# Kernel tuning notes

Hardware: AMD Instinct MI355X
Metric: run time of the kernel (lower is better)

## Reference

```python
import jax, jax.numpy as jnp
import numpy as np

N, E = 100000, 1600000
DIM, H, D = 64, 4, 8          # dim, num_heads, qk_dim
DH = D * H                    # 32
QK_SCALE = (DIM // H) ** -0.5


def setup_inputs() -> dict:
    key = jax.random.key(0)
    k1, k2, k3, k4 = jax.random.split(key, 4)
    x = jax.random.normal(k1, (N, DIM), dtype=jnp.float32)
    edge_index = jax.random.randint(k2, (2, E), 0, N, dtype=jnp.int64)
    W_qkv = jax.random.normal(k3, (DIM, 2 * DH + DIM), dtype=jnp.float32) * (DIM ** -0.5)
    b_qkv = jax.random.normal(k4, (2 * DH + DIM,), dtype=jnp.float32) * 0.02
    return {"x": x, "edge_index": edge_index, "W_qkv": W_qkv, "b_qkv": b_qkv}


def reference(x, edge_index, W_qkv, b_qkv):
    n = x.shape[0]
    e = edge_index.shape[1]
    qkv = x @ W_qkv + b_qkv                       # (N, 2*DH+DIM)
    q = qkv[:, :DH].reshape(n, H, D)
    k = qkv[:, DH:2 * DH].reshape(n, H, D)
    v = qkv[:, 2 * DH:].reshape(n, H, DIM // H)
    s, t = edge_index[0], edge_index[1]
    q_e = q[s] * QK_SCALE                         # (E, H, D)
    k_e = k[t]
    v_e = v[t]                                    # (E, H, DIM/H)
    # scale q by 1/sqrt(num source neighbors) (bincount of s)
    deg = jax.ops.segment_sum(jnp.ones((e,), x.dtype), s, num_segments=n)
    q_e = q_e * (deg[s] ** -0.5)[:, None, None]
    compat = jnp.einsum('ehd,ehd->eh', q_e, k_e)  # (E, H)
    # segment softmax over edges grouped by source node s
    m = jax.ops.segment_max(compat, s, num_segments=n)
    ex = jnp.exp(compat - m[s])
    denom = jax.ops.segment_sum(ex, s, num_segments=n)
    attn = ex / (denom[s] + 1e-16)                # (E, H)
    msg = (v_e * attn[..., None]).reshape(e, DIM)  # (E, DIM)
    out = jax.ops.segment_sum(msg, s, num_segments=n)  # (N, DIM)
    return out
```

## Files before the change

### kernel.cpp

```cpp
#include <hip/hip_runtime.h>


#define NDIM 64
#define NBMAX 1024
#define CTILE 8192
#define STGMAX 4352
#define GEMM_BLKS 316

static __device__ __forceinline__ unsigned short f2bf(float f) {
    unsigned int u = __float_as_uint(f);
    unsigned int r = (u + 0x7fffu + ((u >> 16) & 1u)) >> 16;
    return (unsigned short)r;
}
static __device__ __forceinline__ float bflo(unsigned int u) {
    return __uint_as_float(u << 16);
}
static __device__ __forceinline__ float bfhi(unsigned int u) {
    return __uint_as_float(u & 0xffff0000u);
}

__global__ void fused_bin_gemm_kernel(const int* __restrict__ s_arr,
                                      const int* __restrict__ t_arr,
                                      unsigned int* __restrict__ gcur,
                                      unsigned int* __restrict__ binned,
                                      const float* __restrict__ x,
                                      const float* __restrict__ W,
                                      const float* __restrict__ bvec,
                                      unsigned short* __restrict__ qs16,
                                      unsigned short* __restrict__ kv,
                                      int N, int E, int nbin) {
    __shared__ unsigned int sm[2048];
    int tid = threadIdx.x;

    if (blockIdx.x < (unsigned)nbin) {
        unsigned int* hist  = sm;
        unsigned int* gbase = sm + 1024;
        int e0 = blockIdx.x * CTILE;
        int cnt = min(CTILE, E - e0);

        hist[tid] = 0;
        __syncthreads();
        for (int i = tid; i < cnt; i += 1024)
            atomicAdd(&hist[(unsigned)s_arr[e0 + i] >> 7], 1u);
        __syncthreads();
        {
            unsigned int h = hist[tid];
            gbase[tid] = h
                ? (unsigned)tid * STGMAX + atomicAdd(&gcur[tid], h)
                : 0u;
        }
        __syncthreads();
        for (int i = tid; i < cnt; i += 1024) {
            int s = s_arr[e0 + i];
            int t = t_arr[e0 + i];
            unsigned int bkt = (unsigned)s >> 7;
            unsigned int dst = atomicAdd(&gbase[bkt], 1u);
            if (dst < (bkt + 1u) * STGMAX)
                binned[dst] = ((unsigned)(s & 127) << 17) | (unsigned)t;
        }
    } else {
        float4* xs = (float4*)sm;
        int bid = blockIdx.x - nbin;
        int col = tid & 127;
        int rw  = tid >> 7;
        float w[64];
        #pragma unroll
        for (int k = 0; k < 64; ++k) w[k] = W[k * 128 + col];
        float bias = bvec[col];

        for (int r0 = bid * 8; r0 < N; r0 += GEMM_BLKS * 8) {
            __syncthreads();
            if (tid < 128) {
                int rr = tid >> 4;
                int cc = tid & 15;
                int n = r0 + rr;
                xs[rr * 16 + cc] = (n < N)
                    ? reinterpret_cast<const float4*>(x)[(size_t)n * 16 + cc]
                    : make_float4(0.f, 0.f, 0.f, 0.f);
            }
            __syncthreads();
            int n = r0 + rw;
            if (n < N) {
                float acc = bias;
                #pragma unroll
                for (int k4 = 0; k4 < 16; ++k4) {
                    float4 xv = xs[rw * 16 + k4];
                    acc = fmaf(xv.x, w[4 * k4 + 0], acc);
                    acc = fmaf(xv.y, w[4 * k4 + 1], acc);
                    acc = fmaf(xv.z, w[4 * k4 + 2], acc);
                    acc = fmaf(xv.w, w[4 * k4 + 3], acc);
                }
                if (col < 32) {
                    qs16[(size_t)n * 32 + col] = f2bf(acc);
                } else if (col < 64) {
                    kv[(size_t)n * 96 + (col - 32)] = f2bf(acc);
                } else {
                    kv[(size_t)n * 96 + 32 + (col - 64)] = f2bf(acc);
                }
            }
        }
    }
}

__global__ void __launch_bounds__(512, 8)
sort_aggregate_kernel(const unsigned int* __restrict__ gcur,
                      const unsigned int* __restrict__ binned,
                      const unsigned short* __restrict__ qs16,
                      const unsigned int* __restrict__ kv32,
                      float* __restrict__ out, int N) {
    __shared__ unsigned int hist[128];
    __shared__ unsigned int rstart[128];
    __shared__ unsigned int cur[128];
    __shared__ unsigned int sh[128];
    __shared__ unsigned int stg[STGMAX];

    int b = blockIdx.x;
    int tid = threadIdx.x;
    unsigned int base = (unsigned)b * STGMAX;
    unsigned int cnt = min(gcur[b], (unsigned int)STGMAX);

    if (tid < 128) hist[tid] = 0;
    __syncthreads();
    for (unsigned int i = tid; i < cnt; i += 512)
        atomicAdd(&hist[binned[base + i] >> 17], 1u);
    __syncthreads();

    unsigned int v = (tid < 128) ? hist[tid] : 0;
    unsigned int acc = v;
    if (tid < 128) sh[tid] = acc;
    __syncthreads();
    for (int o = 1; o < 128; o <<= 1) {
        unsigned int add = (tid >= o && tid < 128) ? sh[tid - o] : 0;
        __syncthreads();
        if (tid < 128) { acc += add; sh[tid] = acc; }
        __syncthreads();
    }
    if (tid < 128) {
        unsigned int exc = acc - v;
        rstart[tid] = exc;
        cur[tid] = exc;
    }
    __syncthreads();

    for (unsigned int i = tid; i < cnt; i += 512) {
        unsigned int e = binned[base + i];
        unsigned int p = atomicAdd(&cur[e >> 17], 1u);
        stg[p] = (e & 0x1FFFFu) * 192u;
    }
    __syncthreads();

    int wid = tid >> 6, lane = tid & 63;
    int hl   = lane & 31;
    int sub  = lane >> 5;
    int head = hl >> 3;
    const char* kvb = (const char*)kv32;
    const char* qsb = (const char*)qs16;

    for (int nl = wid * 16; nl < wid * 16 + 16; ++nl) {
        int n = b * 128 + nl;
        if (n >= N) break;
        int dg = (int)hist[nl];
        if (dg == 0) {
            if (lane < 32)
                *reinterpret_cast<float2*>(&out[(size_t)n * 64 + 2 * hl]) =
                    make_float2(0.f, 0.f);
            continue;
        }
        int start = (int)rstart[nl];
        int last = start + dg - 1;
        float sc = 0.25f * rsqrtf((float)dg);

        uint4 q4 = *(const uint4*)(qsb + (size_t)n * 64 + (head << 4));
        float qf0 = bflo(q4.x) * sc, qf1 = bfhi(q4.x) * sc;
        float qf2 = bflo(q4.y) * sc, qf3 = bfhi(q4.y) * sc;
        float qf4 = bflo(q4.z) * sc, qf5 = bfhi(q4.z) * sc;
        float qf6 = bflo(q4.w) * sc, qf7 = bfhi(q4.w) * sc;

        float accx = 0.f, accy = 0.f, den = 0.f;
        int npairs = (dg + 1) >> 1;
        int idx = start + sub;

        unsigned int co = stg[min(idx, last)];
        float wm = (idx <= last) ? 1.f : 0.f;
        uint4 kr = *(const uint4*)(kvb + co + (head << 4));
        unsigned int vr = *(const unsigned int*)(kvb + co + 64 + (hl << 2));

        for (int i = 0; i < npairs; ++i) {
            uint4 kr2 = kr; unsigned int vr2 = vr; float wm2 = 0.f;
            int idx2 = idx + 2;
            if (i + 1 < npairs) {
                unsigned int co2 = stg[min(idx2, last)];
                wm2 = (idx2 <= last) ? 1.f : 0.f;
                kr2 = *(const uint4*)(kvb + co2 + (head << 4));
                vr2 = *(const unsigned int*)(kvb + co2 + 64 + (hl << 2));
            }
            float p = qf0 * bflo(kr.x);
            p = fmaf(qf1, bfhi(kr.x), p);
            p = fmaf(qf2, bflo(kr.y), p);
            p = fmaf(qf3, bfhi(kr.y), p);
            p = fmaf(qf4, bflo(kr.z), p);
            p = fmaf(qf5, bfhi(kr.z), p);
            p = fmaf(qf6, bflo(kr.w), p);
            p = fmaf(qf7, bfhi(kr.w), p);
            float w = __expf(p) * wm;
            accx = fmaf(w, bflo(vr), accx);
            accy = fmaf(w, bfhi(vr), accy);
            den += w;
            kr = kr2; vr = vr2; wm = wm2; idx = idx2;
        }

        accx += __shfl_xor(accx, 32);
        accy += __shfl_xor(accy, 32);
        den  += __shfl_xor(den, 32);

        if (lane < 32) {
            float inv = 1.0f / (den + 1e-16f);
            *reinterpret_cast<float2*>(&out[(size_t)n * 64 + 2 * hl]) =
                make_float2(accx * inv, accy * inv);
        }
    }
}

extern "C" void kernel_launch(void* const* d_in, const int* in_sizes, int n_in,
                              void* d_out, int out_size, void* d_ws, size_t ws_size,
                              hipStream_t stream) {
    const float* x = (const float*)d_in[0];
    const int*   eidx = (const int*)d_in[1];
    const float* W = (const float*)d_in[2];
    const float* b = (const float*)d_in[3];
    int N = in_sizes[0] / NDIM;
    int E = in_sizes[1] / 2;
    float* out = (float*)d_out;

    int NB = (N + 127) / 128;
    int nbin = (E + CTILE - 1) / CTILE;

    unsigned short* qs16 = (unsigned short*)d_ws;
    unsigned short* kv = qs16 + (size_t)N * 32;
    unsigned int* gcur = (unsigned int*)(kv + (size_t)N * 96);
    unsigned int* binned = gcur + NBMAX;

    const int* s_arr = eidx;
    const int* t_arr = eidx + E;

    hipMemsetAsync(gcur, 0, NBMAX * sizeof(unsigned int), stream);

    fused_bin_gemm_kernel<<<nbin + GEMM_BLKS, 1024, 0, stream>>>(
        s_arr, t_arr, gcur, binned, x, W, b, qs16, kv, N, E, nbin);
    sort_aggregate_kernel<<<NB, 512, 0, stream>>>(
        gcur, binned, qs16, (const unsigned int*)kv, out, N);
}
```

Baseline: 183.8 us.

## Split global bin counters into 8 partitions and shrink staging buffer

Binning blocks now write to one of 8 partitions per bucket, chosen by block index, which spreads global atomic contention on the per-bucket counters. Staging capacity per partition is 384 and the aggregate kernel's shared staging array shrinks to 3072 entries to improve occupancy. The scan of bucket counts uses wavefront shuffles instead of a barrier-heavy shared-memory scan. The risk is silently dropped edges when one partition overflows its 384 slots or a bucket exceeds 3072 edges in total.

New measurement: 181.4 us. About the same (-1.3%).

```diff
diff --git a/kernel.cpp b/kernel.cpp
--- a/kernel.cpp
+++ b/kernel.cpp
@@ -4,7 +4,8 @@
 #define NDIM 64
 #define NBMAX 1024
 #define CTILE 8192
-#define STGMAX 4352
+#define STGP 384
+#define STGTOT 3072
 #define GEMM_BLKS 316
 
 static __device__ __forceinline__ unsigned short f2bf(float f) {
@@ -37,6 +38,7 @@
         unsigned int* gbase = sm + 1024;
         int e0 = blockIdx.x * CTILE;
         int cnt = min(CTILE, E - e0);
+        unsigned int part = blockIdx.x & 7u;
 
         hist[tid] = 0;
         __syncthreads();
@@ -45,8 +47,9 @@
         __syncthreads();
         {
             unsigned int h = hist[tid];
+            unsigned int seg = part * (unsigned)NBMAX + (unsigned)tid;
             gbase[tid] = h
-                ? (unsigned)tid * STGMAX + atomicAdd(&gcur[tid], h)
+                ? seg * STGP + atomicAdd(&gcur[seg], h)
                 : 0u;
         }
         __syncthreads();
@@ -55,7 +58,8 @@
             int t = t_arr[e0 + i];
             unsigned int bkt = (unsigned)s >> 7;
             unsigned int dst = atomicAdd(&gbase[bkt], 1u);
-            if (dst < (bkt + 1u) * STGMAX)
+            unsigned int lim = (part * (unsigned)NBMAX + bkt + 1u) * STGP;
+            if (dst < lim)
                 binned[dst] = ((unsigned)(s & 127) << 17) | (unsigned)t;
         }
     } else {
@@ -111,41 +115,54 @@
     __shared__ unsigned int hist[128];
     __shared__ unsigned int rstart[128];
     __shared__ unsigned int cur[128];
-    __shared__ unsigned int sh[128];
-    __shared__ unsigned int stg[STGMAX];
+    __shared__ unsigned int wsum[2];
+    __shared__ unsigned int stg[STGTOT];
 
     int b = blockIdx.x;
     int tid = threadIdx.x;
-    unsigned int base = (unsigned)b * STGMAX;
-    unsigned int cnt = min(gcur[b], (unsigned int)STGMAX);
 
     if (tid < 128) hist[tid] = 0;
     __syncthreads();
-    for (unsigned int i = tid; i < cnt; i += 512)
-        atomicAdd(&hist[binned[base + i] >> 17], 1u);
+    #pragma unroll
+    for (int p = 0; p < 8; ++p) {
+        unsigned int seg = (unsigned)p * NBMAX + (unsigned)b;
+        unsigned int base = seg * STGP;
+        unsigned int cnt = min(gcur[seg], (unsigned int)STGP);
+        for (unsigned int i = tid; i < cnt; i += 512)
+            atomicAdd(&hist[binned[base + i] >> 17], 1u);
+    }
     __syncthreads();
 
-    unsigned int v = (tid < 128) ? hist[tid] : 0;
-    unsigned int acc = v;
-    if (tid < 128) sh[tid] = acc;
-    __syncthreads();
-    for (int o = 1; o < 128; o <<= 1) {
-        unsigned int add = (tid >= o && tid < 128) ? sh[tid - o] : 0;
-        __syncthreads();
-        if (tid < 128) { acc += add; sh[tid] = acc; }
-        __syncthreads();
-    }
-    if (tid < 128) {
-        unsigned int exc = acc - v;
-        rstart[tid] = exc;
-        cur[tid] = exc;
-    }
-    __syncthreads();
-
-    for (unsigned int i = tid; i < cnt; i += 512) {
-        unsigned int e = binned[base + i];
-        unsigned int p = atomicAdd(&cur[e >> 17], 1u);
-        stg[p] = (e & 0x1FFFFu) * 192u;
+    {
+        int lane = tid & 63, wid = tid >> 6;
+        unsigned int v_in = (tid < 128) ? hist[tid] : 0;
+        unsigned int v = v_in;
+        #pragma unroll
+        for (int d = 1; d < 64; d <<= 1) {
+            unsigned int o = __shfl_up(v, d);
+            if (lane >= d) v += o;
+        }
+        if (tid < 128 && lane == 63) wsum[wid] = v;
+        __syncthreads();
+        if (tid < 128) {
+            unsigned int incl = v + ((wid == 1) ? wsum[0] : 0u);
+            unsigned int exc = incl - v_in;
+            rstart[tid] = exc;
+            cur[tid] = exc;
+        }
+        __syncthreads();
+    }
+
+    #pragma unroll
+    for (int p = 0; p < 8; ++p) {
+        unsigned int seg = (unsigned)p * NBMAX + (unsigned)b;
+        unsigned int base = seg * STGP;
+        unsigned int cnt = min(gcur[seg], (unsigned int)STGP);
+        for (unsigned int i = tid; i < cnt; i += 512) {
+            unsigned int e = binned[base + i];
+            unsigned int pp = atomicAdd(&cur[e >> 17], 1u);
+            stg[pp] = (e & 0x1FFFFu) * 192u;
+        }
     }
     __syncthreads();
 
@@ -238,12 +255,12 @@
     unsigned short* qs16 = (unsigned short*)d_ws;
     unsigned short* kv = qs16 + (size_t)N * 32;
     unsigned int* gcur = (unsigned int*)(kv + (size_t)N * 96);
-    unsigned int* binned = gcur + NBMAX;
+    unsigned int* binned = gcur + 8 * NBMAX;
 
     const int* s_arr = eidx;
     const int* t_arr = eidx + E;
 
-    hipMemsetAsync(gcur, 0, NBMAX * sizeof(unsigned int), stream);
+    hipMemsetAsync(gcur, 0, 8 * NBMAX * sizeof(unsigned int), stream);
 
     fused_bin_gemm_kernel<<<nbin + GEMM_BLKS, 1024, 0, stream>>>(
         s_arr, t_arr, gcur, binned, x, W, b, qs16, kv, N, E, nbin);
```
